# Kernel optimization log

Hardware: AMD Instinct MI355X
Metric: run time of the kernel (lower is better)

Reference implementation:

```python
import jax, jax.numpy as jnp
import numpy as np

R = 2
K = 2 * R + 1  # kernel size 5


def _patches(x, axis):
    """Zero-padded sliding-window patches along `axis` for a [B,H,W,1] tensor.
    Mimics tf.image.extract_patches with SAME padding (zeros). Returns [B,H,W,K]."""
    pad = [(0, 0)] * 4
    pad[axis] = (R, R)
    xp = jnp.pad(x, pad)
    n = x.shape[axis]
    slices = [jax.lax.slice_in_dim(xp, i, i + n, axis=axis) for i in range(K)]
    return jnp.concatenate(slices, axis=-1)  # channel dim is 1 -> stacks taps


def _do_blur(bright_p, dark_p, depths_p, depths, spatial_dist, depth_var, spatial_var):
    # depth-guided weight, per tap
    rel = jnp.minimum(jnp.abs(depths_p / depths - 1.0), 1.0)
    w = jnp.exp(-jnp.square(rel) / (2.0 * depth_var)) * \
        jnp.exp(-jnp.square(spatial_dist) / (2.0 * spatial_var))
    w = w / jnp.sum(w, axis=-1, keepdims=True)
    b = jnp.sum(bright_p * w, axis=-1, keepdims=True)
    d = jnp.sum(dark_p * w, axis=-1, keepdims=True)
    return b, d


def _custom_pow(a, b):
    return jnp.exp(b * jnp.log(jnp.maximum(a, 1e-8)))


def setup_inputs() -> dict:
    key = jax.random.key(0)
    k1, k2, k3 = jax.random.split(key, 3)
    B, H, W = 8, 1024, 1024
    bright = jax.random.uniform(k1, (B, H, W, 1), dtype=jnp.float32)
    dark = jax.random.uniform(k2, (B, H, W, 1), dtype=jnp.float32)
    # depths are divided by; keep strictly positive
    depths = 0.1 + 0.9 * jax.random.uniform(k3, (B, H, W, 1), dtype=jnp.float32)
    return {
        "bright": bright,
        "dark": dark,
        "depths": depths,
        "depth_variance": jnp.float32(0.0004),
        "spatial_variance": jnp.float32(13.16),
        "dev_exponent": jnp.float32(0.3),
        "dark_epsilon": jnp.float32(0.375),
        "contrast_enhance": jnp.float32(0.95),
    }


def reference(bright, dark, depths, depth_variance, spatial_variance,
              dev_exponent, dark_epsilon, contrast_enhance):
    spatial_dist = jnp.arange(-R, R + 1, dtype=jnp.float32).reshape(1, 1, 1, K)
    # horizontal pass (along W = axis 2)
    bx, dx, zx = _patches(bright, 2), _patches(dark, 2), _patches(depths, 2)
    bright_x, dark_x = _do_blur(bx, dx, zx, depths, spatial_dist,
                                depth_variance, spatial_variance)
    # vertical pass (along H = axis 1) on horizontally-blurred values
    by, dy, zy = _patches(bright_x, 1), _patches(dark_x, 1), _patches(depths, 1)
    bright_mean, dark_mean = _do_blur(by, dy, zy, depths, spatial_dist,
                                      depth_variance, spatial_variance)
    # contrast-aware blend of bright/dark channels
    dev_bright = _custom_pow(jnp.abs(bright - bright_mean), dev_exponent)
    dev_dark = _custom_pow(jnp.abs(dark - dark_mean), dev_exponent)
    dev_dark = jnp.maximum(dev_dark, dark_epsilon)
    dev_bright = dev_bright * contrast_enhance
    wsum = dev_bright + dev_dark
    dev_bright = dev_bright / wsum
    dev_dark = dev_dark / wsum
    return dev_dark * bright + dev_bright * dark
```

## Files before the change

### kernel.cpp

```cpp
#include <hip/hip_runtime.h>

#define TH 16
#define NIT (TH + 4)

__global__ __launch_bounds__(512, 4)
void bilateral_fused(const float* __restrict__ bright,
                     const float* __restrict__ dark,
                     const float* __restrict__ depths,
                     const float* __restrict__ p_dv,
                     const float* __restrict__ p_sv,
                     const float* __restrict__ p_de,
                     const float* __restrict__ p_deps,
                     const float* __restrict__ p_ce,
                     float* __restrict__ out,
                     int H, int W)
{
    const float LOG2E = 1.44269504088896340736f;
    const float kd  = -LOG2E / (2.0f * p_dv[0]);
    const float ks  = -LOG2E / (2.0f * p_sv[0]);
    const float de  = p_de[0];
    const float dke = p_deps[0];
    const float ce  = p_ce[0];
    const float ks1 = ks;
    const float ks4 = 4.0f * ks;
    const float NEG = -1e30f;

    const int t  = threadIdx.x;
    const int c  = 2 * t;
    const int y0 = blockIdx.y * TH;

    const size_t plane = (size_t)H * W;
    const float* bB = bright + (size_t)blockIdx.z * plane;
    const float* dB = dark   + (size_t)blockIdx.z * plane;
    const float* zB = depths + (size_t)blockIdx.z * plane;
    float*     outB = out    + (size_t)blockIdx.z * plane;

    const int colL = max(c - 2, 0);
    const int colR = min(c + 2, W - 2);

    const float kA0 = (c - 2 >= 0) ? ks4 : NEG;
    const float kA1 = (c - 1 >= 0) ? ks1 : NEG;
    const float kA3 = ks1;
    const float kA4 = (c + 2 <  W) ? ks4 : NEG;
    const float kB0 = (c - 1 >= 0) ? ks4 : NEG;
    const float kB1 = ks1;
    const float kB3 = (c + 2 <  W) ? ks1 : NEG;
    const float kB4 = (c + 3 <  W) ? ks4 : NEG;

    auto wexp = [&](float zp, float invz, float kspat) {
        const float u = fmaf(zp, invz, -1.0f);
        return exp2f(fmaf(u * kd, u, kspat));
    };

    float pb0[5], pb1[5], pd0[5], pd1[5], pz0[5], pz1[5];

#pragma unroll
    for (int i = 0; i < NIT; ++i) {
        const int s  = i % 5;
        const int gy = y0 + i - 2;

        if ((unsigned)gy < (unsigned)H) {
            const size_t ro = (size_t)gy * W;
            const float2 bL = *(const float2*)(bB + ro + colL);
            const float2 bC = *(const float2*)(bB + ro + c);
            const float2 bR = *(const float2*)(bB + ro + colR);
            const float2 dL = *(const float2*)(dB + ro + colL);
            const float2 dC = *(const float2*)(dB + ro + c);
            const float2 dR = *(const float2*)(dB + ro + colR);
            const float2 zL = *(const float2*)(zB + ro + colL);
            const float2 zC = *(const float2*)(zB + ro + c);
            const float2 zR = *(const float2*)(zB + ro + colR);

            const float iA = __builtin_amdgcn_rcpf(zC.x);
            const float w0 = wexp(zL.x, iA, kA0);
            const float w1 = wexp(zL.y, iA, kA1);
            const float w3 = wexp(zC.y, iA, kA3);
            const float w4 = wexp(zR.x, iA, kA4);
            const float wr = __builtin_amdgcn_rcpf(1.0f + w0 + w1 + w3 + w4);
            pb0[s] = fmaf(w0, bL.x, fmaf(w1, bL.y, fmaf(w3, bC.y, fmaf(w4, bR.x, bC.x)))) * wr;
            pd0[s] = fmaf(w0, dL.x, fmaf(w1, dL.y, fmaf(w3, dC.y, fmaf(w4, dR.x, dC.x)))) * wr;
            pz0[s] = zC.x;

            const float iB = __builtin_amdgcn_rcpf(zC.y);
            const float u0 = wexp(zL.y, iB, kB0);
            const float u1 = wexp(zC.x, iB, kB1);
            const float u3 = wexp(zR.x, iB, kB3);
            const float u4 = wexp(zR.y, iB, kB4);
            const float ur = __builtin_amdgcn_rcpf(1.0f + u0 + u1 + u3 + u4);
            pb1[s] = fmaf(u0, bL.y, fmaf(u1, bC.x, fmaf(u3, bR.x, fmaf(u4, bR.y, bC.y)))) * ur;
            pd1[s] = fmaf(u0, dL.y, fmaf(u1, dC.x, fmaf(u3, dR.x, fmaf(u4, dR.y, dC.y)))) * ur;
            pz1[s] = zC.y;
        } else {
            pb0[s] = pb1[s] = pd0[s] = pd1[s] = 0.0f;
            pz0[s] = pz1[s] = 0.0f;
        }

        if (i >= 4) {
            const int orow = y0 + i - 4;
            const int sm2 = (i - 4) % 5, sm1 = (i - 3) % 5, sc = (i - 2) % 5;
            const int sp1 = (i - 1) % 5, sp2 = i % 5;

            const float izA = __builtin_amdgcn_rcpf(pz0[sc]);
            const float v0 = wexp(pz0[sm2], izA, ks4);
            const float v1 = wexp(pz0[sm1], izA, ks1);
            const float v3 = wexp(pz0[sp1], izA, ks1);
            const float v4 = wexp(pz0[sp2], izA, ks4);
            const float vr = __builtin_amdgcn_rcpf(1.0f + v0 + v1 + v3 + v4);
            const float bmA = fmaf(v0, pb0[sm2], fmaf(v1, pb0[sm1], fmaf(v3, pb0[sp1], fmaf(v4, pb0[sp2], pb0[sc])))) * vr;
            const float dmA = fmaf(v0, pd0[sm2], fmaf(v1, pd0[sm1], fmaf(v3, pd0[sp1], fmaf(v4, pd0[sp2], pd0[sc])))) * vr;

            const float izB = __builtin_amdgcn_rcpf(pz1[sc]);
            const float x0 = wexp(pz1[sm2], izB, ks4);
            const float x1 = wexp(pz1[sm1], izB, ks1);
            const float x3 = wexp(pz1[sp1], izB, ks1);
            const float x4 = wexp(pz1[sp2], izB, ks4);
            const float xr = __builtin_amdgcn_rcpf(1.0f + x0 + x1 + x3 + x4);
            const float bmB = fmaf(x0, pb1[sm2], fmaf(x1, pb1[sm1], fmaf(x3, pb1[sp1], fmaf(x4, pb1[sp2], pb1[sc])))) * xr;
            const float dmB = fmaf(x0, pd1[sm2], fmaf(x1, pd1[sm1], fmaf(x3, pd1[sp1], fmaf(x4, pd1[sp2], pd1[sc])))) * xr;

            const size_t oo = (size_t)orow * W + c;
            const float2 bc = *(const float2*)(bB + oo);
            const float2 dc = *(const float2*)(dB + oo);

            const float devbA = exp2f(de * __log2f(fmaxf(fabsf(bc.x - bmA), 1e-8f))) * ce;
            const float devdA = fmaxf(exp2f(de * __log2f(fmaxf(fabsf(dc.x - dmA), 1e-8f))), dke);
            const float wA = __builtin_amdgcn_rcpf(devbA + devdA);
            const float resA = fmaf(devdA, bc.x, devbA * dc.x) * wA;

            const float devbB = exp2f(de * __log2f(fmaxf(fabsf(bc.y - bmB), 1e-8f))) * ce;
            const float devdB = fmaxf(exp2f(de * __log2f(fmaxf(fabsf(dc.y - dmB), 1e-8f))), dke);
            const float wB = __builtin_amdgcn_rcpf(devbB + devdB);
            const float resB = fmaf(devdB, bc.y, devbB * dc.y) * wB;

            *(float2*)(outB + oo) = make_float2(resA, resB);
        }
    }
}

extern "C" void kernel_launch(void* const* d_in, const int* in_sizes, int n_in,
                              void* d_out, int out_size, void* d_ws, size_t ws_size,
                              hipStream_t stream)
{
    const float* bright = (const float*)d_in[0];
    const float* dark   = (const float*)d_in[1];
    const float* depths = (const float*)d_in[2];
    const float* p_dv   = (const float*)d_in[3];
    const float* p_sv   = (const float*)d_in[4];
    const float* p_de   = (const float*)d_in[5];
    const float* p_deps = (const float*)d_in[6];
    const float* p_ce   = (const float*)d_in[7];
    float* out = (float*)d_out;

    const int H = 1024, W = 1024;
    const int B = in_sizes[0] / (H * W);

    dim3 grid(1, H / TH, B);
    dim3 block(512);
    bilateral_fused<<<grid, block, 0, stream>>>(bright, dark, depths,
                                                p_dv, p_sv, p_de, p_deps, p_ce,
                                                out, H, W);
}
```

Before: 170.9 us.

## Process four columns per thread with float4 loads and a partially unrolled row loop

Each thread now covers four adjacent columns with float4 center loads and float2 halos, so halo loads are shared across more outputs. The block shrinks to 256 threads, and the row loop is unrolled five rows at a time with '#pragma unroll 1' around it to keep code size down. Edge taps are masked by setting halo depth to a huge value rather than using per-tap NEG constants, and exp and log now use raw amdgcn builtins. The cost is higher register pressure per thread and fewer threads per block, which halves the total thread count.

```diff
diff --git a/kernel.cpp b/kernel.cpp
--- a/kernel.cpp
+++ b/kernel.cpp
@@ -1,9 +1,110 @@
 #include <hip/hip_runtime.h>
 
 #define TH 16
-#define NIT (TH + 4)
+#define W_ 1024
+#define H_ 1024
 
-__global__ __launch_bounds__(512, 4)
+__device__ __forceinline__ float wexp1(float zp, float iz, float kd, float kspat) {
+    const float u = fmaf(zp, iz, -1.0f);
+    return __builtin_amdgcn_exp2f(fmaf(u * kd, u, kspat));
+}
+
+__device__ __forceinline__ void blur5(
+    float zm2, float zm1, float zc, float zp1, float zp2,
+    float bm2, float bm1, float bc, float bp1, float bp2,
+    float dm2, float dm1, float dc, float dp1, float dp2,
+    float kd, float ks1, float ks4,
+    float& ob, float& od)
+{
+    const float iz = __builtin_amdgcn_rcpf(zc);
+    const float w0 = wexp1(zm2, iz, kd, ks4);
+    const float w1 = wexp1(zm1, iz, kd, ks1);
+    const float w3 = wexp1(zp1, iz, kd, ks1);
+    const float w4 = wexp1(zp2, iz, kd, ks4);
+    const float wr = __builtin_amdgcn_rcpf(1.0f + w0 + w1 + w3 + w4);
+    ob = fmaf(w0, bm2, fmaf(w1, bm1, fmaf(w3, bp1, fmaf(w4, bp2, bc)))) * wr;
+    od = fmaf(w0, dm2, fmaf(w1, dm1, fmaf(w3, dp1, fmaf(w4, dp2, dc)))) * wr;
+}
+
+__device__ __forceinline__ float blend1(float bc, float dc, float bm, float dm,
+                                        float de, float dke, float ce) {
+    const float devb = __builtin_amdgcn_exp2f(
+        de * __builtin_amdgcn_logf(fmaxf(fabsf(bc - bm), 1e-8f))) * ce;
+    const float devd = fmaxf(__builtin_amdgcn_exp2f(
+        de * __builtin_amdgcn_logf(fmaxf(fabsf(dc - dm), 1e-8f))), dke);
+    const float wr = __builtin_amdgcn_rcpf(devb + devd);
+    return fmaf(devd, bc, devb * dc) * wr;
+}
+
+__device__ __forceinline__ void stage_row(
+    int gy, const float* __restrict__ bB, const float* __restrict__ dB,
+    const float* __restrict__ zB,
+    int c, int colL2, int colR2, bool eL, bool eR,
+    float kd, float ks1, float ks4,
+    float4& sb, float4& sd, float4& sz)
+{
+    if ((unsigned)gy < (unsigned)H_) {
+        const size_t ro = (size_t)gy * W_;
+        const float2 lb = *(const float2*)(bB + ro + colL2);
+        const float4 cb = *(const float4*)(bB + ro + c);
+        const float2 rb = *(const float2*)(bB + ro + colR2);
+        const float2 ld = *(const float2*)(dB + ro + colL2);
+        const float4 cd = *(const float4*)(dB + ro + c);
+        const float2 rd = *(const float2*)(dB + ro + colR2);
+        float2 lz = *(const float2*)(zB + ro + colL2);
+        const float4 cz = *(const float4*)(zB + ro + c);
+        float2 rz = *(const float2*)(zB + ro + colR2);
+        if (eL) { lz.x = 1e18f; lz.y = 1e18f; }
+        if (eR) { rz.x = 1e18f; rz.y = 1e18f; }
+        blur5(lz.x, lz.y, cz.x, cz.y, cz.z,  lb.x, lb.y, cb.x, cb.y, cb.z,
+              ld.x, ld.y, cd.x, cd.y, cd.z,  kd, ks1, ks4, sb.x, sd.x);
+        blur5(lz.y, cz.x, cz.y, cz.z, cz.w,  lb.y, cb.x, cb.y, cb.z, cb.w,
+              ld.y, cd.x, cd.y, cd.z, cd.w,  kd, ks1, ks4, sb.y, sd.y);
+        blur5(cz.x, cz.y, cz.z, cz.w, rz.x,  cb.x, cb.y, cb.z, cb.w, rb.x,
+              cd.x, cd.y, cd.z, cd.w, rd.x,  kd, ks1, ks4, sb.z, sd.z);
+        blur5(cz.y, cz.z, cz.w, rz.x, rz.y,  cb.y, cb.z, cb.w, rb.x, rb.y,
+              cd.y, cd.z, cd.w, rd.x, rd.y,  kd, ks1, ks4, sb.w, sd.w);
+        sz = cz;
+    } else {
+        sb = make_float4(0.f, 0.f, 0.f, 0.f);
+        sd = make_float4(0.f, 0.f, 0.f, 0.f);
+        sz = make_float4(0.f, 0.f, 0.f, 0.f);
+    }
+}
+
+#define STEP(S, S0, S1, S2, S3, S4, I)                                        \
+  {                                                                           \
+    stage_row(y0 + (I) - 2, bB, dB, zB, c, colL2, colR2, eL, eR,              \
+              kd, ks1, ks4, pb[S], pd[S], pz[S]);                             \
+    float4 bm, dm;                                                            \
+    blur5(pz[S0].x, pz[S1].x, pz[S2].x, pz[S3].x, pz[S4].x,                   \
+          pb[S0].x, pb[S1].x, pb[S2].x, pb[S3].x, pb[S4].x,                   \
+          pd[S0].x, pd[S1].x, pd[S2].x, pd[S3].x, pd[S4].x,                   \
+          kd, ks1, ks4, bm.x, dm.x);                                          \
+    blur5(pz[S0].y, pz[S1].y, pz[S2].y, pz[S3].y, pz[S4].y,                   \
+          pb[S0].y, pb[S1].y, pb[S2].y, pb[S3].y, pb[S4].y,                   \
+          pd[S0].y, pd[S1].y, pd[S2].y, pd[S3].y, pd[S4].y,                   \
+          kd, ks1, ks4, bm.y, dm.y);                                          \
+    blur5(pz[S0].z, pz[S1].z, pz[S2].z, pz[S3].z, pz[S4].z,                   \
+          pb[S0].z, pb[S1].z, pb[S2].z, pb[S3].z, pb[S4].z,                   \
+          pd[S0].z, pd[S1].z, pd[S2].z, pd[S3].z, pd[S4].z,                   \
+          kd, ks1, ks4, bm.z, dm.z);                                          \
+    blur5(pz[S0].w, pz[S1].w, pz[S2].w, pz[S3].w, pz[S4].w,                   \
+          pb[S0].w, pb[S1].w, pb[S2].w, pb[S3].w, pb[S4].w,                   \
+          pd[S0].w, pd[S1].w, pd[S2].w, pd[S3].w, pd[S4].w,                   \
+          kd, ks1, ks4, bm.w, dm.w);                                          \
+    const size_t oo = (size_t)(y0 + (I) - 4) * W_ + c;                        \
+    const float4 rb4 = *(const float4*)(bB + oo);                             \
+    const float4 rd4 = *(const float4*)(dB + oo);                             \
+    float4 res;                                                               \
+    res.x = blend1(rb4.x, rd4.x, bm.x, dm.x, de, dke, ce);                    \
+    res.y = blend1(rb4.y, rd4.y, bm.y, dm.y, de, dke, ce);                    \
+    res.z = blend1(rb4.z, rd4.z, bm.z, dm.z, de, dke, ce);                    \
+    res.w = blend1(rb4.w, rd4.w, bm.w, dm.w, de, dke, ce);                    \
+    *(float4*)(outB + oo) = res;                                              \
+  }
+
+__global__ __launch_bounds__(256, 2)
 void bilateral_fused(const float* __restrict__ bright,
                      const float* __restrict__ dark,
                      const float* __restrict__ depths,
@@ -12,8 +113,7 @@
                      const float* __restrict__ p_de,
                      const float* __restrict__ p_deps,
                      const float* __restrict__ p_ce,
-                     float* __restrict__ out,
-                     int H, int W)
+                     float* __restrict__ out)
 {
     const float LOG2E = 1.44269504088896340736f;
     const float kd  = -LOG2E / (2.0f * p_dv[0]);
@@ -23,118 +123,40 @@
     const float ce  = p_ce[0];
     const float ks1 = ks;
     const float ks4 = 4.0f * ks;
-    const float NEG = -1e30f;
 
     const int t  = threadIdx.x;
-    const int c  = 2 * t;
+    const int c  = 4 * t;
     const int y0 = blockIdx.y * TH;
 
-    const size_t plane = (size_t)H * W;
+    const size_t plane = (size_t)H_ * W_;
     const float* bB = bright + (size_t)blockIdx.z * plane;
     const float* dB = dark   + (size_t)blockIdx.z * plane;
     const float* zB = depths + (size_t)blockIdx.z * plane;
     float*     outB = out    + (size_t)blockIdx.z * plane;
 
-    const int colL = max(c - 2, 0);
-    const int colR = min(c + 2, W - 2);
+    const int  colL2 = max(c - 2, 0);
+    const int  colR2 = min(c + 4, W_ - 2);
+    const bool eL = (c == 0);
+    const bool eR = (c + 4 >= W_);
 
-    const float kA0 = (c - 2 >= 0) ? ks4 : NEG;
-    const float kA1 = (c - 1 >= 0) ? ks1 : NEG;
-    const float kA3 = ks1;
-    const float kA4 = (c + 2 <  W) ? ks4 : NEG;
-    const float kB0 = (c - 1 >= 0) ? ks4 : NEG;
-    const float kB1 = ks1;
-    const float kB3 = (c + 2 <  W) ? ks1 : NEG;
-    const float kB4 = (c + 3 <  W) ? ks4 : NEG;
+    float4 pb[5], pd[5], pz[5];
 
-    auto wexp = [&](float zp, float invz, float kspat) {
-        const float u = fmaf(zp, invz, -1.0f);
-        return exp2f(fmaf(u * kd, u, kspat));
-    };
+    stage_row(y0 - 2, bB, dB, zB, c, colL2, colR2, eL, eR, kd, ks1, ks4, pb[0], pd[0], pz[0]);
+    stage_row(y0 - 1, bB, dB, zB, c, colL2, colR2, eL, eR, kd, ks1, ks4, pb[1], pd[1], pz[1]);
+    stage_row(y0 + 0, bB, dB, zB, c, colL2, colR2, eL, eR, kd, ks1, ks4, pb[2], pd[2], pz[2]);
+    stage_row(y0 + 1, bB, dB, zB, c, colL2, colR2, eL, eR, kd, ks1, ks4, pb[3], pd[3], pz[3]);
 
-    float pb0[5], pb1[5], pd0[5], pd1[5], pz0[5], pz1[5];
-
-#pragma unroll
-    for (int i = 0; i < NIT; ++i) {
-        const int s  = i % 5;
-        const int gy = y0 + i - 2;
-
-        if ((unsigned)gy < (unsigned)H) {
-            const size_t ro = (size_t)gy * W;
-            const float2 bL = *(const float2*)(bB + ro + colL);
-            const float2 bC = *(const float2*)(bB + ro + c);
-            const float2 bR = *(const float2*)(bB + ro + colR);
-            const float2 dL = *(const float2*)(dB + ro + colL);
-            const float2 dC = *(const float2*)(dB + ro + c);
-            const float2 dR = *(const float2*)(dB + ro + colR);
-            const float2 zL = *(const float2*)(zB + ro + colL);
-            const float2 zC = *(const float2*)(zB + ro + c);
-            const float2 zR = *(const float2*)(zB + ro + colR);
-
-            const float iA = __builtin_amdgcn_rcpf(zC.x);
-            const float w0 = wexp(zL.x, iA, kA0);
-            const float w1 = wexp(zL.y, iA, kA1);
-            const float w3 = wexp(zC.y, iA, kA3);
-            const float w4 = wexp(zR.x, iA, kA4);
-            const float wr = __builtin_amdgcn_rcpf(1.0f + w0 + w1 + w3 + w4);
-            pb0[s] = fmaf(w0, bL.x, fmaf(w1, bL.y, fmaf(w3, bC.y, fmaf(w4, bR.x, bC.x)))) * wr;
-            pd0[s] = fmaf(w0, dL.x, fmaf(w1, dL.y, fmaf(w3, dC.y, fmaf(w4, dR.x, dC.x)))) * wr;
-            pz0[s] = zC.x;
-
-            const float iB = __builtin_amdgcn_rcpf(zC.y);
-            const float u0 = wexp(zL.y, iB, kB0);
-            const float u1 = wexp(zC.x, iB, kB1);
-            const float u3 = wexp(zR.x, iB, kB3);
-            const float u4 = wexp(zR.y, iB, kB4);
-            const float ur = __builtin_amdgcn_rcpf(1.0f + u0 + u1 + u3 + u4);
-            pb1[s] = fmaf(u0, bL.y, fmaf(u1, bC.x, fmaf(u3, bR.x, fmaf(u4, bR.y, bC.y)))) * ur;
-            pd1[s] = fmaf(u0, dL.y, fmaf(u1, dC.x, fmaf(u3, dR.x, fmaf(u4, dR.y, dC.y)))) * ur;
-            pz1[s] = zC.y;
-        } else {
-            pb0[s] = pb1[s] = pd0[s] = pd1[s] = 0.0f;
-            pz0[s] = pz1[s] = 0.0f;
-        }
-
-        if (i >= 4) {
-            const int orow = y0 + i - 4;
-            const int sm2 = (i - 4) % 5, sm1 = (i - 3) % 5, sc = (i - 2) % 5;
-            const int sp1 = (i - 1) % 5, sp2 = i % 5;
-
-            const float izA = __builtin_amdgcn_rcpf(pz0[sc]);
-            const float v0 = wexp(pz0[sm2], izA, ks4);
-            const float v1 = wexp(pz0[sm1], izA, ks1);
-            const float v3 = wexp(pz0[sp1], izA, ks1);
-            const float v4 = wexp(pz0[sp2], izA, ks4);
-            const float vr = __builtin_amdgcn_rcpf(1.0f + v0 + v1 + v3 + v4);
-            const float bmA = fmaf(v0, pb0[sm2], fmaf(v1, pb0[sm1], fmaf(v3, pb0[sp1], fmaf(v4, pb0[sp2], pb0[sc])))) * vr;
-            const float dmA = fmaf(v0, pd0[sm2], fmaf(v1, pd0[sm1], fmaf(v3, pd0[sp1], fmaf(v4, pd0[sp2], pd0[sc])))) * vr;
-
-            const float izB = __builtin_amdgcn_rcpf(pz1[sc]);
-            const float x0 = wexp(pz1[sm2], izB, ks4);
-            const float x1 = wexp(pz1[sm1], izB, ks1);
-            const float x3 = wexp(pz1[sp1], izB, ks1);
-            const float x4 = wexp(pz1[sp2], izB, ks4);
-            const float xr = __builtin_amdgcn_rcpf(1.0f + x0 + x1 + x3 + x4);
-            const float bmB = fmaf(x0, pb1[sm2], fmaf(x1, pb1[sm1], fmaf(x3, pb1[sp1], fmaf(x4, pb1[sp2], pb1[sc])))) * xr;
-            const float dmB = fmaf(x0, pd1[sm2], fmaf(x1, pd1[sm1], fmaf(x3, pd1[sp1], fmaf(x4, pd1[sp2], pd1[sc])))) * xr;
-
-            const size_t oo = (size_t)orow * W + c;
-            const float2 bc = *(const float2*)(bB + oo);
-            const float2 dc = *(const float2*)(dB + oo);
-
-            const float devbA = exp2f(de * __log2f(fmaxf(fabsf(bc.x - bmA), 1e-8f))) * ce;
-            const float devdA = fmaxf(exp2f(de * __log2f(fmaxf(fabsf(dc.x - dmA), 1e-8f))), dke);
-            const float wA = __builtin_amdgcn_rcpf(devbA + devdA);
-            const float resA = fmaf(devdA, bc.x, devbA * dc.x) * wA;
-
-            const float devbB = exp2f(de * __log2f(fmaxf(fabsf(bc.y - bmB), 1e-8f))) * ce;
-            const float devdB = fmaxf(exp2f(de * __log2f(fmaxf(fabsf(dc.y - dmB), 1e-8f))), dke);
-            const float wB = __builtin_amdgcn_rcpf(devbB + devdB);
-            const float resB = fmaf(devdB, bc.y, devbB * dc.y) * wB;
-
-            *(float2*)(outB + oo) = make_float2(resA, resB);
-        }
+    int i = 4;
+#pragma unroll 1
+    for (int it = 0; it < 3; ++it) {
+        STEP(4, 0, 1, 2, 3, 4, i + 0)
+        STEP(0, 1, 2, 3, 4, 0, i + 1)
+        STEP(1, 2, 3, 4, 0, 1, i + 2)
+        STEP(2, 3, 4, 0, 1, 2, i + 3)
+        STEP(3, 4, 0, 1, 2, 3, i + 4)
+        i += 5;
     }
+    STEP(4, 0, 1, 2, 3, 4, 19)
 }
 
 extern "C" void kernel_launch(void* const* d_in, const int* in_sizes, int n_in,
@@ -151,12 +173,11 @@
     const float* p_ce   = (const float*)d_in[7];
     float* out = (float*)d_out;
 
-    const int H = 1024, W = 1024;
-    const int B = in_sizes[0] / (H * W);
+    const int B = in_sizes[0] / (H_ * W_);
 
-    dim3 grid(1, H / TH, B);
-    dim3 block(512);
+    dim3 grid(1, H_ / TH, B);
+    dim3 block(256);
     bilateral_fused<<<grid, block, 0, stream>>>(bright, dark, depths,
                                                 p_dv, p_sv, p_de, p_deps, p_ce,
-                                                out, H, W);
+                                                out);
 }
```

Result: faster. 161.5 us (-5.5%).
